# Kernel tuning notes

Hardware: AMD Instinct MI355X
Metric: run time of the kernel (lower is better)

Reference implementation:

```python
import jax, jax.numpy as jnp
import numpy as np

DIM = 1024
NUM_HEADS = 16
HEAD_DIM = DIM // NUM_HEADS
BATCH = 2
SEQ = 2048


def setup_inputs() -> dict:
    key = jax.random.key(0)
    ks = jax.random.split(key, 9)
    s = 1.0 / np.sqrt(DIM)  # torch Linear default init scale
    x = jax.random.normal(ks[0], (BATCH, SEQ, DIM), dtype=jnp.float32)
    Wq = jax.random.uniform(ks[1], (DIM, DIM), jnp.float32, -s, s)
    bq = jax.random.uniform(ks[2], (DIM,), jnp.float32, -s, s)
    Wk = jax.random.uniform(ks[3], (DIM, DIM), jnp.float32, -s, s)
    bk = jax.random.uniform(ks[4], (DIM,), jnp.float32, -s, s)
    Wv = jax.random.uniform(ks[5], (DIM, DIM), jnp.float32, -s, s)
    bv = jax.random.uniform(ks[6], (DIM,), jnp.float32, -s, s)
    Wo = jax.random.uniform(ks[7], (DIM, DIM), jnp.float32, -s, s)
    bo = jax.random.uniform(ks[8], (DIM,), jnp.float32, -s, s)
    return {"x": x, "Wq": Wq, "bq": bq, "Wk": Wk, "bk": bk,
            "Wv": Wv, "bv": bv, "Wo": Wo, "bo": bo, "enable_causal": 1}


def reference(x, Wq, bq, Wk, bk, Wv, bv, Wo, bo, enable_causal):
    B, S, D = x.shape
    H, Hd = NUM_HEADS, HEAD_DIM
    # projections (torch Linear: x @ W.T + b; W here stored as [out,in])
    q = (x @ Wq.T + bq).reshape(B, S, H, Hd).transpose(0, 2, 1, 3)  # [B,H,S,Hd]
    k = (x @ Wk.T + bk).reshape(B, S, H, Hd).transpose(0, 2, 1, 3)
    v = (x @ Wv.T + bv).reshape(B, S, H, Hd).transpose(0, 2, 1, 3)
    scores = jnp.einsum('bhqd,bhkd->bhqk', q, k) / np.sqrt(Hd)  # [B,H,S,S]
    if enable_causal:
        causal = jnp.triu(jnp.ones((S, S), dtype=bool), k=1)
        scores = jnp.where(causal, -jnp.inf, scores)
    attn = jax.nn.softmax(scores, axis=-1)
    # dropout p=0.0 -> identity (eval-mode math)
    out = jnp.einsum('bhqk,bhkd->bhqd', attn, v)  # [B,H,S,Hd]
    out = out.transpose(0, 2, 1, 3).reshape(B, S, D)
    return out @ Wo.T + bo
```

## Files before the change

### kernel.cpp

```cpp
#include <hip/hip_runtime.h>
#include <hip/hip_bf16.h>
#include <stdint.h>

typedef unsigned short u16;
typedef short bf16x8 __attribute__((ext_vector_type(8)));
typedef float f32x4 __attribute__((ext_vector_type(4)));

#define S_LEN   2048
#define D_MODEL 1024
#define NH      16
#define M_TOK   4096
#define LOG2E   1.4426950408889634f

__device__ __forceinline__ u16 f2b(float f) {
  union { float f; unsigned int u; } v; v.f = f;
  unsigned int r = v.u + 0x7FFFu + ((v.u >> 16) & 1u);
  return (u16)(r >> 16);
}

__device__ __forceinline__ float exp2_fast(float x) {
  float r;
  asm("v_exp_f32 %0, %1" : "=v"(r) : "v"(x));
  return r;
}

__device__ __forceinline__ void load_lds16(const void* g, void* l) {
  __builtin_amdgcn_global_load_lds(
      (const __attribute__((address_space(1))) void*)g,
      (__attribute__((address_space(3))) void*)l, 16, 0, 0);
}

__global__ __launch_bounds__(256) void k_convert(
    const float* __restrict__ x,
    const float* __restrict__ wq, const float* __restrict__ wk,
    const float* __restrict__ wv, const float* __restrict__ wo,
    u16* __restrict__ xb, u16* __restrict__ wb)
{
  int t = blockIdx.x * 256 + threadIdx.x;
  long e = (long)t * 8;
  const float* src; u16* dst;
  if (e < (long)M_TOK * D_MODEL) { src = x + e; dst = xb + e; }
  else {
    long we = e - (long)M_TOK * D_MODEL;
    int r = (int)(we >> 20);
    long o = we & 1048575;
    const float* ws = (r == 0) ? wq : (r == 1) ? wk : (r == 2) ? wv : wo;
    src = ws + o; dst = wb + ((long)r << 20) + o;
  }
  float4 f0 = *(const float4*)src;
  float4 f1 = *(const float4*)(src + 4);
  u16 u[8];
  u[0] = f2b(f0.x); u[1] = f2b(f0.y); u[2] = f2b(f0.z); u[3] = f2b(f0.w);
  u[4] = f2b(f1.x); u[5] = f2b(f1.y); u[6] = f2b(f1.z); u[7] = f2b(f1.w);
  *(uint4*)dst = *(const uint4*)u;
}

__device__ __forceinline__ void gemm_mainloop(
    const u16* __restrict__ At, const u16* __restrict__ Bt,
    u16* As, u16* Bs, f32x4 acc[4][4])
{
  const int tid  = threadIdx.x;
  const int lane = tid & 63;
  const int w    = tid >> 6;
  const int wr = w >> 1, wc = w & 1;
  const f32x4 fz = {0.f, 0.f, 0.f, 0.f};
  #pragma unroll
  for (int i = 0; i < 4; ++i)
    #pragma unroll
    for (int j = 0; j < 4; ++j) acc[i][j] = fz;

  const int srow = lane >> 3;
  const int sc   = lane & 7;

  for (int k0 = 0; k0 < D_MODEL; k0 += 64) {
    #pragma unroll
    for (int i = 0; i < 4; ++i) {
      int seg = i * 4 + w;
      int row = seg * 8 + srow;
      load_lds16(At + (long)row * D_MODEL + k0 + sc * 8, (char*)As + seg * 1024);
      load_lds16(Bt + (long)row * D_MODEL + k0 + sc * 8, (char*)Bs + seg * 1024);
    }
    __syncthreads();
    #pragma unroll
    for (int kc = 0; kc < 2; ++kc) {
      bf16x8 af[4], bfv[4];
      #pragma unroll
      for (int mi = 0; mi < 4; ++mi) {
        int row = wr * 64 + mi * 16 + (lane & 15);
        af[mi] = *(const bf16x8*)(As + row * 64 + kc * 32 + (lane >> 4) * 8);
      }
      #pragma unroll
      for (int ni = 0; ni < 4; ++ni) {
        int row = wc * 64 + ni * 16 + (lane & 15);
        bfv[ni] = *(const bf16x8*)(Bs + row * 64 + kc * 32 + (lane >> 4) * 8);
      }
      #pragma unroll
      for (int mi = 0; mi < 4; ++mi)
        #pragma unroll
        for (int ni = 0; ni < 4; ++ni)
          acc[mi][ni] = __builtin_amdgcn_mfma_f32_16x16x32_bf16(
              af[mi], bfv[ni], acc[mi][ni], 0, 0, 0);
    }
    __syncthreads();
  }
}

__global__ __launch_bounds__(256) void k_gemm_qkv(
    const u16* __restrict__ xb, const u16* __restrict__ wb,
    const float* __restrict__ bq, const float* __restrict__ bk,
    const float* __restrict__ bv,
    u16* __restrict__ q, u16* __restrict__ k, u16* __restrict__ v)
{
  __shared__ u16 As[128 * 64];
  __shared__ u16 Bs[128 * 64];
  const int m0   = blockIdx.x * 128;
  const int by   = blockIdx.y;
  const int proj = by >> 3;
  const int n0   = (by & 7) * 128;
  f32x4 acc[4][4];
  gemm_mainloop(xb + (long)m0 * D_MODEL,
                wb + (long)proj * 1048576 + (long)n0 * D_MODEL, As, Bs, acc);

  const int lane = threadIdx.x & 63;
  const int w    = threadIdx.x >> 6;
  const int wr = w >> 1, wc = w & 1;
  const float* bias = (proj == 0) ? bq : (proj == 1) ? bk : bv;
  u16* dst = (proj == 0) ? q : (proj == 1) ? k : v;
  const float sc = (proj == 0) ? 0.125f * LOG2E : 1.0f;
  #pragma unroll
  for (int mi = 0; mi < 4; ++mi)
    #pragma unroll
    for (int ni = 0; ni < 4; ++ni) {
      int n = n0 + wc * 64 + ni * 16 + (lane & 15);
      float bval = bias[n];
      int h = n >> 6, d = n & 63;
      #pragma unroll
      for (int r = 0; r < 4; ++r) {
        int m = m0 + wr * 64 + mi * 16 + (lane >> 4) * 4 + r;
        int b = m >> 11, s = m & 2047;
        float val = (acc[mi][ni][r] + bval) * sc;
        dst[(((long)(b * NH + h) * S_LEN + s) << 6) + d] = f2b(val);
      }
    }
}

__global__ __launch_bounds__(256) void k_transpose_v(
    const u16* __restrict__ v, u16* __restrict__ vt)
{
  __shared__ u16 t[64][65];
  const int bh = blockIdx.y;
  const int s0 = blockIdx.x * 64;
  const int tid = threadIdx.x;
  const int r = tid >> 2, cg = tid & 3;
  const u16* src = v + ((long)bh * S_LEN + s0 + r) * 64 + cg * 16;
  uint4 a = *(const uint4*)src;
  uint4 b = *(const uint4*)(src + 8);
  u16 tmp[16];
  *(uint4*)tmp = a; *(uint4*)(tmp + 8) = b;
  #pragma unroll
  for (int j = 0; j < 16; ++j) t[r][cg * 16 + j] = tmp[j];
  __syncthreads();
  u16 o[16];
  #pragma unroll
  for (int j = 0; j < 16; ++j) o[j] = t[cg * 16 + j][r];
  u16* dst = vt + ((long)bh * 64 + r) * S_LEN + s0 + cg * 16;
  *(uint4*)dst = *(const uint4*)o;
  *(uint4*)(dst + 8) = *(const uint4*)(o + 8);
}

__global__ __launch_bounds__(256) void k_attn(
    const u16* __restrict__ Q, const u16* __restrict__ K,
    const u16* __restrict__ Vt, u16* __restrict__ O,
    const int* __restrict__ causal_flag)
{
  __shared__ u16 Ks[2][64 * 64];
  __shared__ u16 Ps[4][16 * 72];

  const int tid  = threadIdx.x;
  const int lane = tid & 63;
  const int w    = tid >> 6;
  const int bid  = blockIdx.x;
  const int xcd  = bid & 7;
  const int j    = bid >> 3;
  const int kk   = j >> 5;
  const int c    = j & 31;
  const int bh   = xcd * 4 + kk;
  const int cc   = (kk & 2) ? ((c + 16) & 31) : c;
  const int qb   = (kk & 1) ? (31 - cc) : cc;
  const int q0   = qb * 64;
  const int causal = *causal_flag;

  const int l15 = lane & 15;
  const int l4  = lane >> 4;

  const u16* Kbh  = K  + (long)bh * S_LEN * 64;
  const u16* Vtbh = Vt + (long)bh * 64 * S_LEN;
  const f32x4 fz = {0.f, 0.f, 0.f, 0.f};
  const int nt = causal ? (qb + 1) : (S_LEN / 64);

  bf16x8 onesv;
  #pragma unroll
  for (int i = 0; i < 8; ++i) onesv[i] = (short)0x3F80;

  const u16 *kg0, *kg1; int lo0, lo1;
  {
    int b0 = w * 64;
    int r0 = (b0 >> 3) + (lane >> 3);
    int c0 = (lane & 7) ^ (r0 & 7);
    kg0 = Kbh + r0 * 64 + c0 * 8;  lo0 = b0 * 16;
    int b1 = 256 + w * 64;
    int r1 = (b1 >> 3) + (lane >> 3);
    int c1 = (lane & 7) ^ (r1 & 7);
    kg1 = Kbh + r1 * 64 + c1 * 8;  lo1 = b1 * 16;
  }
  #define STAGE_T(bufp, toff) do {                                   \
    load_lds16(kg0 + (toff) * 4096, (char*)(bufp) + lo0);            \
    load_lds16(kg1 + (toff) * 4096, (char*)(bufp) + lo1);            \
  } while (0)

  const u16* Vp0 = Vtbh + (long)( 0 + l15) * S_LEN + l4 * 8;
  const u16* Vp1 = Vtbh + (long)(16 + l15) * S_LEN + l4 * 8;
  const u16* Vp2 = Vtbh + (long)(32 + l15) * S_LEN + l4 * 8;
  const u16* Vp3 = Vtbh + (long)(48 + l15) * S_LEN + l4 * 8;

  const u16* Qb = Q + ((long)bh * S_LEN + q0 + w * 16) * 64;
  bf16x8 qf0 = *(const bf16x8*)(Qb + l15 * 64 +      l4 * 8);
  bf16x8 qf1 = *(const bf16x8*)(Qb + l15 * 64 + 32 + l4 * 8);

  f32x4 acc_o[4] = {fz, fz, fz, fz};
  f32x4 acc_l = fz;

  int cur = 0;
  STAGE_T(Ks[0], 0);
  asm volatile("s_waitcnt vmcnt(0)" ::: "memory");
  __builtin_amdgcn_s_barrier();

  #pragma unroll 1
  for (int t = 0; t < nt; ++t) {
    bf16x8 vf0[4], vf1[4];
    vf0[0] = *(const bf16x8*)(Vp0); vf1[0] = *(const bf16x8*)(Vp0 + 32);
    vf0[1] = *(const bf16x8*)(Vp1); vf1[1] = *(const bf16x8*)(Vp1 + 32);
    vf0[2] = *(const bf16x8*)(Vp2); vf1[2] = *(const bf16x8*)(Vp2 + 32);
    vf0[3] = *(const bf16x8*)(Vp3); vf1[3] = *(const bf16x8*)(Vp3 + 32);

    if (t + 1 < nt) STAGE_T(Ks[cur ^ 1], t + 1);

    f32x4 acc_s[4] = {fz, fz, fz, fz};
    __builtin_amdgcn_s_setprio(1);
    #pragma unroll
    for (int kc = 0; kc < 2; ++kc) {
      bf16x8 qf = kc ? qf1 : qf0;
      #pragma unroll
      for (int sub = 0; sub < 4; ++sub) {
        int krow = sub * 16 + l15;
        int cs = (kc * 4 + l4) ^ (krow & 7);
        bf16x8 kf = *(const bf16x8*)(Ks[cur] + krow * 64 + cs * 8);
        acc_s[sub] = __builtin_amdgcn_mfma_f32_16x16x32_bf16(qf, kf, acc_s[sub], 0, 0, 0);
      }
    }
    __builtin_amdgcn_s_setprio(0);

    if (causal && t == nt - 1) {
      #pragma unroll
      for (int sub = 0; sub < 4; ++sub) {
        int kvcol = t * 64 + sub * 16 + l15;
        #pragma unroll
        for (int r = 0; r < 4; ++r) {
          int qrow = q0 + w * 16 + l4 * 4 + r;
          if (kvcol > qrow) acc_s[sub][r] = -1e30f;
        }
      }
    }

    u16* P = &Ps[w][0];
    #pragma unroll
    for (int sub = 0; sub < 4; ++sub)
      #pragma unroll
      for (int r = 0; r < 4; ++r) {
        float p = exp2_fast(acc_s[sub][r]);
        P[(l4 * 4 + r) * 72 + sub * 16 + l15] = f2b(p);
      }

    asm volatile("s_waitcnt lgkmcnt(0)" ::: "memory");
    bf16x8 pf0 = *(const bf16x8*)(P + l15 * 72 +      l4 * 8);
    bf16x8 pf1 = *(const bf16x8*)(P + l15 * 72 + 32 + l4 * 8);
    __builtin_amdgcn_s_setprio(1);
    #pragma unroll
    for (int sub = 0; sub < 4; ++sub) {
      acc_o[sub] = __builtin_amdgcn_mfma_f32_16x16x32_bf16(pf0, vf0[sub], acc_o[sub], 0, 0, 0);
      acc_o[sub] = __builtin_amdgcn_mfma_f32_16x16x32_bf16(pf1, vf1[sub], acc_o[sub], 0, 0, 0);
    }
    acc_l = __builtin_amdgcn_mfma_f32_16x16x32_bf16(pf0, onesv, acc_l, 0, 0, 0);
    acc_l = __builtin_amdgcn_mfma_f32_16x16x32_bf16(pf1, onesv, acc_l, 0, 0, 0);
    __builtin_amdgcn_s_setprio(0);

    if (t + 1 < nt) {
      asm volatile("s_waitcnt vmcnt(0)" ::: "memory");
      __builtin_amdgcn_s_barrier();
      cur ^= 1;
    }
    Vp0 += 64; Vp1 += 64; Vp2 += 64; Vp3 += 64;
  }
  #undef STAGE_T

  const int b = bh >> 4, h = bh & 15;
  float rl[4];
  #pragma unroll
  for (int r = 0; r < 4; ++r) {
    asm("v_rcp_f32 %0, %1" : "=v"(rl[r]) : "v"(acc_l[r]));
  }
  #pragma unroll
  for (int sub = 0; sub < 4; ++sub)
    #pragma unroll
    for (int r = 0; r < 4; ++r) {
      int s = q0 + w * 16 + l4 * 4 + r;
      float val = acc_o[sub][r] * rl[r];
      O[((long)(b * S_LEN + s)) * D_MODEL + h * 64 + sub * 16 + l15] = f2b(val);
    }
}

__global__ __launch_bounds__(256) void k_gemm_o(
    const u16* __restrict__ ob, const u16* __restrict__ wb,
    const float* __restrict__ bo, float* __restrict__ out)
{
  __shared__ u16 As[128 * 64];
  __shared__ u16 Bs[128 * 64];
  const int m0 = blockIdx.x * 128;
  const int n0 = blockIdx.y * 128;
  f32x4 acc[4][4];
  gemm_mainloop(ob + (long)m0 * D_MODEL,
                wb + 3L * 1048576 + (long)n0 * D_MODEL, As, Bs, acc);
  const int lane = threadIdx.x & 63;
  const int w    = threadIdx.x >> 6;
  const int wr = w >> 1, wc = w & 1;
  #pragma unroll
  for (int mi = 0; mi < 4; ++mi)
    #pragma unroll
    for (int ni = 0; ni < 4; ++ni) {
      int n = n0 + wc * 64 + ni * 16 + (lane & 15);
      float bval = bo[n];
      #pragma unroll
      for (int r = 0; r < 4; ++r) {
        int m = m0 + wr * 64 + mi * 16 + (lane >> 4) * 4 + r;
        out[(long)m * D_MODEL + n] = acc[mi][ni][r] + bval;
      }
    }
}

extern "C" void kernel_launch(void* const* d_in, const int* in_sizes, int n_in,
                              void* d_out, int out_size, void* d_ws, size_t ws_size,
                              hipStream_t stream) {
  const float* x  = (const float*)d_in[0];
  const float* Wq = (const float*)d_in[1];
  const float* bq = (const float*)d_in[2];
  const float* Wk = (const float*)d_in[3];
  const float* bk = (const float*)d_in[4];
  const float* Wv = (const float*)d_in[5];
  const float* bv = (const float*)d_in[6];
  const float* Wo = (const float*)d_in[7];
  const float* bo = (const float*)d_in[8];
  const int* causal = (const int*)d_in[9];
  float* out = (float*)d_out;

  char* ws = (char*)d_ws;
  u16* xb = (u16*)(ws);
  u16* wb = (u16*)(ws + (8L  << 20));
  u16* qb = (u16*)(ws + (16L << 20));
  u16* kb = (u16*)(ws + (24L << 20));
  u16* vb = (u16*)(ws + (32L << 20));
  u16* vt = (u16*)(ws + (40L << 20));
  u16* ob = (u16*)(ws);

  k_convert   <<<4096,          256, 0, stream>>>(x, Wq, Wk, Wv, Wo, xb, wb);
  k_gemm_qkv  <<<dim3(32, 24),  256, 0, stream>>>(xb, wb, bq, bk, bv, qb, kb, vb);
  k_transpose_v<<<dim3(32, 32), 256, 0, stream>>>(vb, vt);
  k_attn      <<<1024,          256, 0, stream>>>(qb, kb, vt, ob, causal);
  k_gemm_o    <<<dim3(32, 8),   256, 0, stream>>>(ob, wb, bo, out);
}
```

Before: 251.3 us.

## Double-buffer GEMM LDS, fuse V transpose into QKV epilogue, pair causal attention blocks

The shared GEMM mainloop now double-buffers its A/B LDS tiles, so the next K-slice loads while MFMAs run on the current one. The QKV epilogue writes V directly in transposed layout with 4-element vector stores, which removes the separate transpose kernel and its round trip through memory. The attention kernel now runs 512 blocks, and each block handles two query tiles (qx and 31-qx) so causal work is balanced per block. In exchange the GEMM uses twice the LDS, and fewer, longer attention blocks may lower occupancy or tail behaviour.

```diff
diff --git a/kernel.cpp b/kernel.cpp
--- a/kernel.cpp
+++ b/kernel.cpp
@@ -72,27 +72,47 @@
   const int srow = lane >> 3;
   const int sc   = lane & 7;
 
+  const u16 *Ag[4], *Bg[4];
+  int ldsoff[4];
+  #pragma unroll
+  for (int i = 0; i < 4; ++i) {
+    int seg = i * 4 + w;
+    int row = seg * 8 + srow;
+    Ag[i] = At + (long)row * D_MODEL + sc * 8;
+    Bg[i] = Bt + (long)row * D_MODEL + sc * 8;
+    ldsoff[i] = seg * 1024;
+  }
+
+  #define GSTAGE(buf, k0_) do {                                              \
+    _Pragma("unroll")                                                        \
+    for (int i_ = 0; i_ < 4; ++i_) {                                         \
+      load_lds16(Ag[i_] + (k0_), (char*)As + (buf) * 16384 + ldsoff[i_]);    \
+      load_lds16(Bg[i_] + (k0_), (char*)Bs + (buf) * 16384 + ldsoff[i_]);    \
+    }                                                                        \
+  } while (0)
+
+  int cur = 0;
+  GSTAGE(0, 0);
+  asm volatile("s_waitcnt vmcnt(0)" ::: "memory");
+  __builtin_amdgcn_s_barrier();
+
   for (int k0 = 0; k0 < D_MODEL; k0 += 64) {
-    #pragma unroll
-    for (int i = 0; i < 4; ++i) {
-      int seg = i * 4 + w;
-      int row = seg * 8 + srow;
-      load_lds16(At + (long)row * D_MODEL + k0 + sc * 8, (char*)As + seg * 1024);
-      load_lds16(Bt + (long)row * D_MODEL + k0 + sc * 8, (char*)Bs + seg * 1024);
-    }
-    __syncthreads();
+    if (k0 + 64 < D_MODEL) GSTAGE(cur ^ 1, k0 + 64);
+
+    const u16* Ab = As + cur * 8192;
+    const u16* Bb = Bs + cur * 8192;
     #pragma unroll
     for (int kc = 0; kc < 2; ++kc) {
       bf16x8 af[4], bfv[4];
       #pragma unroll
       for (int mi = 0; mi < 4; ++mi) {
         int row = wr * 64 + mi * 16 + (lane & 15);
-        af[mi] = *(const bf16x8*)(As + row * 64 + kc * 32 + (lane >> 4) * 8);
+        af[mi] = *(const bf16x8*)(Ab + row * 64 + kc * 32 + (lane >> 4) * 8);
       }
       #pragma unroll
       for (int ni = 0; ni < 4; ++ni) {
         int row = wc * 64 + ni * 16 + (lane & 15);
-        bfv[ni] = *(const bf16x8*)(Bs + row * 64 + kc * 32 + (lane >> 4) * 8);
+        bfv[ni] = *(const bf16x8*)(Bb + row * 64 + kc * 32 + (lane >> 4) * 8);
       }
       #pragma unroll
       for (int mi = 0; mi < 4; ++mi)
@@ -101,18 +121,24 @@
           acc[mi][ni] = __builtin_amdgcn_mfma_f32_16x16x32_bf16(
               af[mi], bfv[ni], acc[mi][ni], 0, 0, 0);
     }
-    __syncthreads();
-  }
+
+    if (k0 + 64 < D_MODEL) {
+      asm volatile("s_waitcnt vmcnt(0)" ::: "memory");
+      __builtin_amdgcn_s_barrier();
+      cur ^= 1;
+    }
+  }
+  #undef GSTAGE
 }
 
 __global__ __launch_bounds__(256) void k_gemm_qkv(
     const u16* __restrict__ xb, const u16* __restrict__ wb,
     const float* __restrict__ bq, const float* __restrict__ bk,
     const float* __restrict__ bv,
-    u16* __restrict__ q, u16* __restrict__ k, u16* __restrict__ v)
+    u16* __restrict__ q, u16* __restrict__ k, u16* __restrict__ vt)
 {
-  __shared__ u16 As[128 * 64];
-  __shared__ u16 Bs[128 * 64];
+  __shared__ u16 As[2 * 128 * 64];
+  __shared__ u16 Bs[2 * 128 * 64];
   const int m0   = blockIdx.x * 128;
   const int by   = blockIdx.y;
   const int proj = by >> 3;
@@ -125,47 +151,41 @@
   const int w    = threadIdx.x >> 6;
   const int wr = w >> 1, wc = w & 1;
   const float* bias = (proj == 0) ? bq : (proj == 1) ? bk : bv;
-  u16* dst = (proj == 0) ? q : (proj == 1) ? k : v;
   const float sc = (proj == 0) ? 0.125f * LOG2E : 1.0f;
-  #pragma unroll
-  for (int mi = 0; mi < 4; ++mi)
-    #pragma unroll
-    for (int ni = 0; ni < 4; ++ni) {
-      int n = n0 + wc * 64 + ni * 16 + (lane & 15);
-      float bval = bias[n];
-      int h = n >> 6, d = n & 63;
-      #pragma unroll
-      for (int r = 0; r < 4; ++r) {
-        int m = m0 + wr * 64 + mi * 16 + (lane >> 4) * 4 + r;
+
+  if (proj == 2) {
+    #pragma unroll
+    for (int mi = 0; mi < 4; ++mi)
+      #pragma unroll
+      for (int ni = 0; ni < 4; ++ni) {
+        int n = n0 + wc * 64 + ni * 16 + (lane & 15);
+        float bval = bias[n];
+        int h = n >> 6, d = n & 63;
+        int m = m0 + wr * 64 + mi * 16 + (lane >> 4) * 4;
         int b = m >> 11, s = m & 2047;
-        float val = (acc[mi][ni][r] + bval) * sc;
-        dst[(((long)(b * NH + h) * S_LEN + s) << 6) + d] = f2b(val);
-      }
-    }
-}
-
-__global__ __launch_bounds__(256) void k_transpose_v(
-    const u16* __restrict__ v, u16* __restrict__ vt)
-{
-  __shared__ u16 t[64][65];
-  const int bh = blockIdx.y;
-  const int s0 = blockIdx.x * 64;
-  const int tid = threadIdx.x;
-  const int r = tid >> 2, cg = tid & 3;
-  const u16* src = v + ((long)bh * S_LEN + s0 + r) * 64 + cg * 16;
-  uint4 a = *(const uint4*)src;
-  uint4 b = *(const uint4*)(src + 8);
-  u16 tmp[16];
-  *(uint4*)tmp = a; *(uint4*)(tmp + 8) = b;
-  #pragma unroll
-  for (int j = 0; j < 16; ++j) t[r][cg * 16 + j] = tmp[j];
-  __syncthreads();
-  u16 o[16];
-  #pragma unroll
-  for (int j = 0; j < 16; ++j) o[j] = t[cg * 16 + j][r];
-  u16* dst = vt + ((long)bh * 64 + r) * S_LEN + s0 + cg * 16;
-  *(uint4*)dst = *(const uint4*)o;
-  *(uint4*)(dst + 8) = *(const uint4*)(o + 8);
+        u16 o4[4];
+        #pragma unroll
+        for (int r = 0; r < 4; ++r) o4[r] = f2b(acc[mi][ni][r] + bval);
+        *(uint2*)&vt[((long)(b * NH + h) * 64 + d) * S_LEN + s] = *(uint2*)o4;
+      }
+  } else {
+    u16* dst = (proj == 0) ? q : k;
+    #pragma unroll
+    for (int mi = 0; mi < 4; ++mi)
+      #pragma unroll
+      for (int ni = 0; ni < 4; ++ni) {
+        int n = n0 + wc * 64 + ni * 16 + (lane & 15);
+        float bval = bias[n];
+        int h = n >> 6, d = n & 63;
+        #pragma unroll
+        for (int r = 0; r < 4; ++r) {
+          int m = m0 + wr * 64 + mi * 16 + (lane >> 4) * 4 + r;
+          int b = m >> 11, s = m & 2047;
+          float val = (acc[mi][ni][r] + bval) * sc;
+          dst[(((long)(b * NH + h) * S_LEN + s) << 6) + d] = f2b(val);
+        }
+      }
+  }
 }
 
 __global__ __launch_bounds__(256) void k_attn(
@@ -182,12 +202,8 @@
   const int bid  = blockIdx.x;
   const int xcd  = bid & 7;
   const int j    = bid >> 3;
-  const int kk   = j >> 5;
-  const int c    = j & 31;
-  const int bh   = xcd * 4 + kk;
-  const int cc   = (kk & 2) ? ((c + 16) & 31) : c;
-  const int qb   = (kk & 1) ? (31 - cc) : cc;
-  const int q0   = qb * 64;
+  const int bh   = xcd * 4 + (j >> 4);
+  const int qx   = j & 15;
   const int causal = *causal_flag;
 
   const int l15 = lane & 15;
@@ -196,7 +212,6 @@
   const u16* Kbh  = K  + (long)bh * S_LEN * 64;
   const u16* Vtbh = Vt + (long)bh * 64 * S_LEN;
   const f32x4 fz = {0.f, 0.f, 0.f, 0.f};
-  const int nt = causal ? (qb + 1) : (S_LEN / 64);
 
   bf16x8 onesv;
   #pragma unroll
@@ -218,113 +233,122 @@
     load_lds16(kg1 + (toff) * 4096, (char*)(bufp) + lo1);            \
   } while (0)
 
-  const u16* Vp0 = Vtbh + (long)( 0 + l15) * S_LEN + l4 * 8;
-  const u16* Vp1 = Vtbh + (long)(16 + l15) * S_LEN + l4 * 8;
-  const u16* Vp2 = Vtbh + (long)(32 + l15) * S_LEN + l4 * 8;
-  const u16* Vp3 = Vtbh + (long)(48 + l15) * S_LEN + l4 * 8;
-
-  const u16* Qb = Q + ((long)bh * S_LEN + q0 + w * 16) * 64;
-  bf16x8 qf0 = *(const bf16x8*)(Qb + l15 * 64 +      l4 * 8);
-  bf16x8 qf1 = *(const bf16x8*)(Qb + l15 * 64 + 32 + l4 * 8);
-
-  f32x4 acc_o[4] = {fz, fz, fz, fz};
-  f32x4 acc_l = fz;
-
-  int cur = 0;
-  STAGE_T(Ks[0], 0);
-  asm volatile("s_waitcnt vmcnt(0)" ::: "memory");
-  __builtin_amdgcn_s_barrier();
-
   #pragma unroll 1
-  for (int t = 0; t < nt; ++t) {
-    bf16x8 vf0[4], vf1[4];
-    vf0[0] = *(const bf16x8*)(Vp0); vf1[0] = *(const bf16x8*)(Vp0 + 32);
-    vf0[1] = *(const bf16x8*)(Vp1); vf1[1] = *(const bf16x8*)(Vp1 + 32);
-    vf0[2] = *(const bf16x8*)(Vp2); vf1[2] = *(const bf16x8*)(Vp2 + 32);
-    vf0[3] = *(const bf16x8*)(Vp3); vf1[3] = *(const bf16x8*)(Vp3 + 32);
-
-    if (t + 1 < nt) STAGE_T(Ks[cur ^ 1], t + 1);
-
-    f32x4 acc_s[4] = {fz, fz, fz, fz};
-    __builtin_amdgcn_s_setprio(1);
-    #pragma unroll
-    for (int kc = 0; kc < 2; ++kc) {
-      bf16x8 qf = kc ? qf1 : qf0;
+  for (int half = 0; half < 2; ++half) {
+    const int qb = half ? (31 - qx) : qx;
+    const int q0 = qb * 64;
+    const int nt = causal ? (qb + 1) : (S_LEN / 64);
+
+    const u16* Qb = Q + ((long)bh * S_LEN + q0 + w * 16) * 64;
+    bf16x8 qf0 = *(const bf16x8*)(Qb + l15 * 64 +      l4 * 8);
+    bf16x8 qf1 = *(const bf16x8*)(Qb + l15 * 64 + 32 + l4 * 8);
+
+    const u16* Vp0 = Vtbh + (long)( 0 + l15) * S_LEN + l4 * 8;
+    const u16* Vp1 = Vtbh + (long)(16 + l15) * S_LEN + l4 * 8;
+    const u16* Vp2 = Vtbh + (long)(32 + l15) * S_LEN + l4 * 8;
+    const u16* Vp3 = Vtbh + (long)(48 + l15) * S_LEN + l4 * 8;
+
+    f32x4 acc_o[4] = {fz, fz, fz, fz};
+    f32x4 acc_l = fz;
+
+    if (half) __builtin_amdgcn_s_barrier();
+
+    int cur = 0;
+    STAGE_T(Ks[0], 0);
+    asm volatile("s_waitcnt vmcnt(0)" ::: "memory");
+    __builtin_amdgcn_s_barrier();
+
+    #pragma unroll 1
+    for (int t = 0; t < nt; ++t) {
+      bf16x8 vf0[4], vf1[4];
+      vf0[0] = *(const bf16x8*)(Vp0); vf1[0] = *(const bf16x8*)(Vp0 + 32);
+      vf0[1] = *(const bf16x8*)(Vp1); vf1[1] = *(const bf16x8*)(Vp1 + 32);
+      vf0[2] = *(const bf16x8*)(Vp2); vf1[2] = *(const bf16x8*)(Vp2 + 32);
+      vf0[3] = *(const bf16x8*)(Vp3); vf1[3] = *(const bf16x8*)(Vp3 + 32);
+
+      if (t + 1 < nt) STAGE_T(Ks[cur ^ 1], t + 1);
+
+      f32x4 acc_s[4] = {fz, fz, fz, fz};
+      __builtin_amdgcn_s_setprio(1);
+      #pragma unroll
+      for (int kc = 0; kc < 2; ++kc) {
+        bf16x8 qf = kc ? qf1 : qf0;
+        #pragma unroll
+        for (int sub = 0; sub < 4; ++sub) {
+          int krow = sub * 16 + l15;
+          int cs = (kc * 4 + l4) ^ (krow & 7);
+          bf16x8 kf = *(const bf16x8*)(Ks[cur] + krow * 64 + cs * 8);
+          acc_s[sub] = __builtin_amdgcn_mfma_f32_16x16x32_bf16(qf, kf, acc_s[sub], 0, 0, 0);
+        }
+      }
+      __builtin_amdgcn_s_setprio(0);
+
+      if (causal && t == nt - 1) {
+        #pragma unroll
+        for (int sub = 0; sub < 4; ++sub) {
+          int kvcol = t * 64 + sub * 16 + l15;
+          #pragma unroll
+          for (int r = 0; r < 4; ++r) {
+            int qrow = q0 + w * 16 + l4 * 4 + r;
+            if (kvcol > qrow) acc_s[sub][r] = -1e30f;
+          }
+        }
+      }
+
+      u16* P = &Ps[w][0];
+      #pragma unroll
+      for (int sub = 0; sub < 4; ++sub)
+        #pragma unroll
+        for (int r = 0; r < 4; ++r) {
+          float p = exp2_fast(acc_s[sub][r]);
+          P[(l4 * 4 + r) * 72 + sub * 16 + l15] = f2b(p);
+        }
+
+      asm volatile("s_waitcnt lgkmcnt(0)" ::: "memory");
+      bf16x8 pf0 = *(const bf16x8*)(P + l15 * 72 +      l4 * 8);
+      bf16x8 pf1 = *(const bf16x8*)(P + l15 * 72 + 32 + l4 * 8);
+      __builtin_amdgcn_s_setprio(1);
       #pragma unroll
       for (int sub = 0; sub < 4; ++sub) {
-        int krow = sub * 16 + l15;
-        int cs = (kc * 4 + l4) ^ (krow & 7);
-        bf16x8 kf = *(const bf16x8*)(Ks[cur] + krow * 64 + cs * 8);
-        acc_s[sub] = __builtin_amdgcn_mfma_f32_16x16x32_bf16(qf, kf, acc_s[sub], 0, 0, 0);
-      }
+        acc_o[sub] = __builtin_amdgcn_mfma_f32_16x16x32_bf16(pf0, vf0[sub], acc_o[sub], 0, 0, 0);
+        acc_o[sub] = __builtin_amdgcn_mfma_f32_16x16x32_bf16(pf1, vf1[sub], acc_o[sub], 0, 0, 0);
+      }
+      acc_l = __builtin_amdgcn_mfma_f32_16x16x32_bf16(pf0, onesv, acc_l, 0, 0, 0);
+      acc_l = __builtin_amdgcn_mfma_f32_16x16x32_bf16(pf1, onesv, acc_l, 0, 0, 0);
+      __builtin_amdgcn_s_setprio(0);
+
+      if (t + 1 < nt) {
+        asm volatile("s_waitcnt vmcnt(0)" ::: "memory");
+        __builtin_amdgcn_s_barrier();
+        cur ^= 1;
+      }
+      Vp0 += 64; Vp1 += 64; Vp2 += 64; Vp3 += 64;
     }
-    __builtin_amdgcn_s_setprio(0);
-
-    if (causal && t == nt - 1) {
-      #pragma unroll
-      for (int sub = 0; sub < 4; ++sub) {
-        int kvcol = t * 64 + sub * 16 + l15;
-        #pragma unroll
-        for (int r = 0; r < 4; ++r) {
-          int qrow = q0 + w * 16 + l4 * 4 + r;
-          if (kvcol > qrow) acc_s[sub][r] = -1e30f;
-        }
-      }
+
+    const int b = bh >> 4, h = bh & 15;
+    float rl[4];
+    #pragma unroll
+    for (int r = 0; r < 4; ++r) {
+      asm("v_rcp_f32 %0, %1" : "=v"(rl[r]) : "v"(acc_l[r]));
     }
-
-    u16* P = &Ps[w][0];
     #pragma unroll
     for (int sub = 0; sub < 4; ++sub)
       #pragma unroll
       for (int r = 0; r < 4; ++r) {
-        float p = exp2_fast(acc_s[sub][r]);
-        P[(l4 * 4 + r) * 72 + sub * 16 + l15] = f2b(p);
-      }
-
-    asm volatile("s_waitcnt lgkmcnt(0)" ::: "memory");
-    bf16x8 pf0 = *(const bf16x8*)(P + l15 * 72 +      l4 * 8);
-    bf16x8 pf1 = *(const bf16x8*)(P + l15 * 72 + 32 + l4 * 8);
-    __builtin_amdgcn_s_setprio(1);
-    #pragma unroll
-    for (int sub = 0; sub < 4; ++sub) {
-      acc_o[sub] = __builtin_amdgcn_mfma_f32_16x16x32_bf16(pf0, vf0[sub], acc_o[sub], 0, 0, 0);
-      acc_o[sub] = __builtin_amdgcn_mfma_f32_16x16x32_bf16(pf1, vf1[sub], acc_o[sub], 0, 0, 0);
-    }
-    acc_l = __builtin_amdgcn_mfma_f32_16x16x32_bf16(pf0, onesv, acc_l, 0, 0, 0);
-    acc_l = __builtin_amdgcn_mfma_f32_16x16x32_bf16(pf1, onesv, acc_l, 0, 0, 0);
-    __builtin_amdgcn_s_setprio(0);
-
-    if (t + 1 < nt) {
-      asm volatile("s_waitcnt vmcnt(0)" ::: "memory");
-      __builtin_amdgcn_s_barrier();
-      cur ^= 1;
-    }
-    Vp0 += 64; Vp1 += 64; Vp2 += 64; Vp3 += 64;
+        int s = q0 + w * 16 + l4 * 4 + r;
+        float val = acc_o[sub][r] * rl[r];
+        O[((long)(b * S_LEN + s)) * D_MODEL + h * 64 + sub * 16 + l15] = f2b(val);
+      }
   }
   #undef STAGE_T
-
-  const int b = bh >> 4, h = bh & 15;
-  float rl[4];
-  #pragma unroll
-  for (int r = 0; r < 4; ++r) {
-    asm("v_rcp_f32 %0, %1" : "=v"(rl[r]) : "v"(acc_l[r]));
-  }
-  #pragma unroll
-  for (int sub = 0; sub < 4; ++sub)
-    #pragma unroll
-    for (int r = 0; r < 4; ++r) {
-      int s = q0 + w * 16 + l4 * 4 + r;
-      float val = acc_o[sub][r] * rl[r];
-      O[((long)(b * S_LEN + s)) * D_MODEL + h * 64 + sub * 16 + l15] = f2b(val);
-    }
 }
 
 __global__ __launch_bounds__(256) void k_gemm_o(
     const u16* __restrict__ ob, const u16* __restrict__ wb,
     const float* __restrict__ bo, float* __restrict__ out)
 {
-  __shared__ u16 As[128 * 64];
-  __shared__ u16 Bs[128 * 64];
+  __shared__ u16 As[2 * 128 * 64];
+  __shared__ u16 Bs[2 * 128 * 64];
   const int m0 = blockIdx.x * 128;
   const int n0 = blockIdx.y * 128;
   f32x4 acc[4][4];
@@ -367,13 +391,11 @@
   u16* wb = (u16*)(ws + (8L  << 20));
   u16* qb = (u16*)(ws + (16L << 20));
   u16* kb = (u16*)(ws + (24L << 20));
-  u16* vb = (u16*)(ws + (32L << 20));
-  u16* vt = (u16*)(ws + (40L << 20));
+  u16* vt = (u16*)(ws + (32L << 20));
   u16* ob = (u16*)(ws);
 
   k_convert   <<<4096,          256, 0, stream>>>(x, Wq, Wk, Wv, Wo, xb, wb);
-  k_gemm_qkv  <<<dim3(32, 24),  256, 0, stream>>>(xb, wb, bq, bk, bv, qb, kb, vb);
-  k_transpose_v<<<dim3(32, 32), 256, 0, stream>>>(vb, vt);
-  k_attn      <<<1024,          256, 0, stream>>>(qb, kb, vt, ob, causal);
+  k_gemm_qkv  <<<dim3(32, 24),  256, 0, stream>>>(xb, wb, bq, bk, bv, qb, kb, vt);
+  k_attn      <<<512,           256, 0, stream>>>(qb, kb, vt, ob, causal);
   k_gemm_o    <<<dim3(32, 8),   256, 0, stream>>>(ob, wb, bo, out);
 }
```

Result: faster. 240.0 us (-4.5%).
